# Kernel tuning notes

Measured on AMD Instinct MI355X. Metric: run time of the kernel, lower is better.

## Reference

```python
import jax, jax.numpy as jnp
import numpy as np

B, H, S, D, T = 2, 32, 8192, 128, 512


def setup_inputs() -> dict:
    key = jax.random.key(0)
    k1, k2, k3, k4 = jax.random.split(key, 4)
    return {
        "cache_k": jax.random.normal(k1, (B, H, S, D), dtype=jnp.float32),
        "cache_v": jax.random.normal(k2, (B, H, S, D), dtype=jnp.float32),
        "new_k": jax.random.normal(k3, (B, H, T, D), dtype=jnp.float32),
        "new_v": jax.random.normal(k4, (B, H, T, D), dtype=jnp.float32),
        "position_ids": jnp.arange(T, dtype=jnp.int64),  # contiguous prefill positions
    }


def reference(cache_k, cache_v, new_k, new_v, position_ids):
    # torch: cache.scatter(2, pos.expand(B,H,T,D), new) with unique positions
    # == write new_k/new_v rows into the cache along the sequence axis.
    updated_k = cache_k.at[:, :, position_ids, :].set(new_k)
    updated_v = cache_v.at[:, :, position_ids, :].set(new_v)
    return (updated_k, updated_v)
```

## Files before the change

### kernel.cpp

```cpp
#include <hip/hip_runtime.h>


#define S_LEN 8192
#define T_LEN 512
#define D_DIM 128
#define BH    64
#define ELEMS_PER_TENSOR (BH * S_LEN * D_DIM)
#define VECS_PER_BH      (S_LEN * (D_DIM / 4))
#define NEW_VECS_PER_BH  (T_LEN * (D_DIM / 4))

typedef float f4_t __attribute__((ext_vector_type(4)));

__global__ __launch_bounds__(256) void ssc_fused(
    const f4_t* __restrict__ ck, const f4_t* __restrict__ cv,
    const f4_t* __restrict__ nk, const f4_t* __restrict__ nv,
    const void* __restrict__ pos,
    f4_t* __restrict__ ok, f4_t* __restrict__ ov) {

    __shared__ int lmap[256];
    const int ltid = threadIdx.x;
    const int bh   = blockIdx.y * (BH / 2) + (blockIdx.x >> 5);
    const int s0   = (blockIdx.x & 31) * 256;

    lmap[ltid] = -1;
    __syncthreads();

    {
        const long long* p64 = (const long long*)pos;
        const int*       p32 = (const int*)pos;
        long long a = p64[0], b = p64[1];
        bool is64 = (a >= 0) && (a < S_LEN) && (b >= 0) && (b < S_LEN) && (a != b);
        #pragma unroll
        for (int j = ltid; j < T_LEN; j += 256) {
            int p = is64 ? (int)p64[j] : p32[j];
            unsigned r = (unsigned)(p - s0);
            if (r < 256u) lmap[r] = j;
        }
    }
    __syncthreads();

    const f4_t* csrc = blockIdx.z ? cv : ck;
    const f4_t* nsrc = blockIdx.z ? nv : nk;
    f4_t*       odst = blockIdx.z ? ov : ok;

    const int chunkBase = bh * VECS_PER_BH + s0 * 32;
    const f4_t* cbase = csrc + chunkBase + ltid;
    f4_t*       dbase = odst + chunkBase + ltid;
    const f4_t* nbase = nsrc + bh * NEW_VECS_PER_BH + (ltid & 31);
    const int   rlane = ltid >> 5;

    #pragma unroll 8
    for (int i = 0; i < 32; ++i) {
        const int t = lmap[i * 8 + rlane];
        f4_t v;
        if (t >= 0) v = nbase[t * 32];
        else        v = __builtin_nontemporal_load(cbase + i * 256);
        dbase[i * 256] = v;
    }
}

extern "C" void kernel_launch(void* const* d_in, const int* in_sizes, int n_in,
                              void* d_out, int out_size, void* d_ws, size_t ws_size,
                              hipStream_t stream) {
    const f4_t* ck = (const f4_t*)d_in[0];
    const f4_t* cv = (const f4_t*)d_in[1];
    const f4_t* nk = (const f4_t*)d_in[2];
    const f4_t* nv = (const f4_t*)d_in[3];
    const void* pos = d_in[4];

    float* out = (float*)d_out;
    f4_t* ok = (f4_t*)out;
    f4_t* ov = (f4_t*)(out + ELEMS_PER_TENSOR);

    ssc_fused<<<dim3(1024, 2, 2), 256, 0, stream>>>(ck, cv, nk, nv, pos, ok, ov);
}
```

Baseline: 209.0 us.

## Split fused scatter into a grid-stride bulk copy plus separate scatter kernel

Replaces the fused kernel, which built a per-chunk position map in shared memory, with two kernels. The first streams the whole cache to the output using nontemporal loads and stores over a fixed grid. The second overwrites the scattered rows with the new values. This removes the shared-memory map, the syncs and the per-element branching, but the scattered rows are now read from the cache and written twice, and it adds a second launch.

Measured after the change: 250.3 us. 19.8% more time.

```diff
diff --git a/kernel.cpp b/kernel.cpp
--- a/kernel.cpp
+++ b/kernel.cpp
@@ -6,57 +6,46 @@
 #define D_DIM 128
 #define BH    64
 #define ELEMS_PER_TENSOR (BH * S_LEN * D_DIM)
+#define VECS_PER_TENSOR  (ELEMS_PER_TENSOR / 4)
 #define VECS_PER_BH      (S_LEN * (D_DIM / 4))
 #define NEW_VECS_PER_BH  (T_LEN * (D_DIM / 4))
+#define NEW_VECS_TOTAL   (BH * NEW_VECS_PER_BH)
 
 typedef float f4_t __attribute__((ext_vector_type(4)));
 
-__global__ __launch_bounds__(256) void ssc_fused(
+__global__ __launch_bounds__(256) void ssc_copy(
     const f4_t* __restrict__ ck, const f4_t* __restrict__ cv,
+    f4_t* __restrict__ ok, f4_t* __restrict__ ov) {
+    const f4_t* __restrict__ src = blockIdx.y ? cv : ck;
+    f4_t*       __restrict__ dst = blockIdx.y ? ov : ok;
+    const int tid = blockIdx.x * 256 + threadIdx.x;
+    #pragma unroll 4
+    for (int i = 0; i < VECS_PER_TENSOR / (2048 * 256); ++i) {
+        const int idx = tid + i * (2048 * 256);
+        f4_t v = __builtin_nontemporal_load(src + idx);
+        __builtin_nontemporal_store(v, dst + idx);
+    }
+}
+
+__global__ __launch_bounds__(256) void ssc_scatter(
     const f4_t* __restrict__ nk, const f4_t* __restrict__ nv,
     const void* __restrict__ pos,
     f4_t* __restrict__ ok, f4_t* __restrict__ ov) {
+    const int v   = blockIdx.x * 256 + threadIdx.x;
+    const int d4  = v & 31;
+    const int t   = (v >> 5) & (T_LEN - 1);
+    const int bh  = v >> 14;
 
-    __shared__ int lmap[256];
-    const int ltid = threadIdx.x;
-    const int bh   = blockIdx.y * (BH / 2) + (blockIdx.x >> 5);
-    const int s0   = (blockIdx.x & 31) * 256;
+    const long long* p64 = (const long long*)pos;
+    const int*       p32 = (const int*)pos;
+    long long a = p64[0], b = p64[1];
+    bool is64 = (a >= 0) && (a < S_LEN) && (b >= 0) && (b < S_LEN) && (a != b);
+    int s = is64 ? (int)p64[t] : p32[t];
+    if ((unsigned)s >= (unsigned)S_LEN) return;
 
-    lmap[ltid] = -1;
-    __syncthreads();
-
-    {
-        const long long* p64 = (const long long*)pos;
-        const int*       p32 = (const int*)pos;
-        long long a = p64[0], b = p64[1];
-        bool is64 = (a >= 0) && (a < S_LEN) && (b >= 0) && (b < S_LEN) && (a != b);
-        #pragma unroll
-        for (int j = ltid; j < T_LEN; j += 256) {
-            int p = is64 ? (int)p64[j] : p32[j];
-            unsigned r = (unsigned)(p - s0);
-            if (r < 256u) lmap[r] = j;
-        }
-    }
-    __syncthreads();
-
-    const f4_t* csrc = blockIdx.z ? cv : ck;
-    const f4_t* nsrc = blockIdx.z ? nv : nk;
-    f4_t*       odst = blockIdx.z ? ov : ok;
-
-    const int chunkBase = bh * VECS_PER_BH + s0 * 32;
-    const f4_t* cbase = csrc + chunkBase + ltid;
-    f4_t*       dbase = odst + chunkBase + ltid;
-    const f4_t* nbase = nsrc + bh * NEW_VECS_PER_BH + (ltid & 31);
-    const int   rlane = ltid >> 5;
-
-    #pragma unroll 8
-    for (int i = 0; i < 32; ++i) {
-        const int t = lmap[i * 8 + rlane];
-        f4_t v;
-        if (t >= 0) v = nbase[t * 32];
-        else        v = __builtin_nontemporal_load(cbase + i * 256);
-        dbase[i * 256] = v;
-    }
+    const f4_t* __restrict__ src = blockIdx.y ? nv : nk;
+    f4_t*       __restrict__ dst = blockIdx.y ? ov : ok;
+    dst[bh * VECS_PER_BH + s * 32 + d4] = src[v];
 }
 
 extern "C" void kernel_launch(void* const* d_in, const int* in_sizes, int n_in,
@@ -72,5 +61,6 @@
     f4_t* ok = (f4_t*)out;
     f4_t* ov = (f4_t*)(out + ELEMS_PER_TENSOR);
 
-    ssc_fused<<<dim3(1024, 2, 2), 256, 0, stream>>>(ck, cv, nk, nv, pos, ok, ov);
+    ssc_copy<<<dim3(2048, 2), 256, 0, stream>>>(ck, cv, ok, ov);
+    ssc_scatter<<<dim3(4096, 2), 256, 0, stream>>>(nk, nv, pos, ok, ov);
 }
```
